# Kernel optimization log

Hardware: AMD Instinct MI355X
Metric: run time of the kernel (lower is better)

Reference implementation:

```python
import jax, jax.numpy as jnp
import numpy as np

DT = 0.1
DEATH_THRESHOLD = 0.05


def setup_inputs() -> dict:
    key = jax.random.key(0)
    ks = jax.random.split(key, 12)
    B, S, DE, DM, DC, DEPTH = 1, 4096, 256, 64, 64, 4
    DIN = DE + DC
    w_scale = 0.02  # keeps pre-softmax scores in a sane range
    return {
        "e": jax.random.normal(ks[0], (B, S, DE), jnp.float32),
        "E": jax.random.uniform(ks[1], (B, S, 1), jnp.float32),
        "P": jax.random.uniform(ks[2], (B, S, 1), jnp.float32),
        "G": jax.random.normal(ks[3], (B, S, 1), jnp.float32),
        "m": jax.random.uniform(ks[4], (B, S, DM), jnp.float32),
        "c": jax.random.normal(ks[5], (B, S, DC), jnp.float32),
        "l": jax.random.uniform(ks[6], (B, S, 1), jnp.float32),
        "wq": jax.random.normal(ks[7], (DEPTH, DIN, DE), jnp.float32) * w_scale,
        "bq": jnp.zeros((DEPTH, DE), jnp.float32),
        "wk": jax.random.normal(ks[8], (DEPTH, DIN, DE), jnp.float32) * w_scale,
        "bk": jnp.zeros((DEPTH, DE), jnp.float32),
        "wv": jax.random.normal(ks[9], (DEPTH, DIN, DE), jnp.float32) * w_scale,
        "bv": jnp.zeros((DEPTH, DE), jnp.float32),
        "alpha": jnp.full((DEPTH,), 1.0, jnp.float32),
        "beta": jnp.full((DEPTH,), 0.5, jnp.float32),
        "gamma": jnp.full((DEPTH,), 0.2, jnp.float32),
        "basal": jnp.full((DEPTH,), 0.05, jnp.float32),
    }


def reference(e, E, P, G, m, c, l, wq, bq, wk, bk, wv, bv, alpha, beta, gamma, basal):
    depth = wq.shape[0]
    scale = 1.0 / np.sqrt(wq.shape[-1]).astype(np.float32)
    for i in range(depth):
        # --- OuterTrans: multiplicatively-masked self-attention ---
        x = jnp.concatenate([e, c], axis=-1)                 # [B,S,DE+DC]
        q = x @ wq[i] + bq[i]
        k = x @ wk[i] + bk[i]
        v = x @ wv[i] + bv[i]
        scores = jnp.einsum("bsd,btd->bst", q, k) * scale    # [B,S,S]
        membrane = jnp.einsum("bsd,btd->bst", m, m)          # [B,S,S]
        lifespan = jnp.einsum("bsd,btd->bst", l, l)          # [B,S,S]
        attn = jax.nn.softmax(scores * membrane * lifespan, axis=-1)
        h_tilde = jnp.einsum("bst,btd->bsd", attn, v)        # [B,S,DE]
        e = e + h_tilde
        # --- ThermodynamicODE (elementwise per-token update) ---
        S_in = jnp.sum(h_tilde * h_tilde, axis=-1, keepdims=True)  # ||h||^2 [B,S,1]
        PE = P * E
        P_new = jax.nn.relu(P + (alpha[i] * S_in - beta[i] * PE) * DT)
        E_new = jax.nn.relu(E + (basal[i] - gamma[i] * PE) * DT)
        m_target = jax.nn.sigmoid(E_new - P_new)             # [B,S,1] broadcast to m
        G = G + (0.1 * E_new - 0.5 * P_new) * DT
        l_decay = 0.01 + 0.5 * jax.nn.relu(P_new - 2.0)
        m = 0.9 * m + 0.1 * m_target
        l = jnp.clip(l - l_decay * DT, 0.0, 1.0)
        E, P = E_new, P_new
    # Dynamic pruning: jit-compatible variant -> zero-mask dead cells instead of
    # data-dependent slicing; also return alive_mask and num_died.
    alive = l > DEATH_THRESHOLD                              # [B,S,1] bool
    af = alive.astype(e.dtype)
    num_died = e.shape[1] - jnp.sum(alive.astype(jnp.int32))
    return (e * af, E * af, P * af, G * af, m * af, c * af, l * af,
            alive[0, :, 0], num_died)
```

## Files before the change

### kernel.cpp

```cpp
#include <hip/hip_runtime.h>
#include <hip/hip_bf16.h>
#include <math.h>

#define SS 4096
#define DE 256
#define DM 64
#define DC 64
#define DIN 320
#define DEPTH 4
#define DT_C 0.1f
#define NSPLIT 12
#define BK 32
#define EXP_SHIFT 8.0f

typedef float f32x4_t __attribute__((ext_vector_type(4)));
typedef __bf16 bf16x8_t __attribute__((ext_vector_type(8)));

#define MFMA_BF16(A, B, C) __builtin_amdgcn_mfma_f32_16x16x32_bf16((A), (B), (C), 0, 0, 0)

#define OFF_E     (SS*DE)
#define OFF_P     (OFF_E + SS)
#define OFF_G     (OFF_P + SS)
#define OFF_M     (OFF_G + SS)
#define OFF_C     (OFF_M + SS*DM)
#define OFF_L     (OFF_C + SS*DM)
#define OFF_ALIVE (OFF_L + SS)
#define OFF_DIED  (OFF_ALIVE + SS)

#define WS_EWS   0
#define WS_MWS   (WS_EWS  + SS*DE)
#define WS_EE    (WS_MWS  + SS*DM)
#define WS_PP    (WS_EE   + SS)
#define WS_GG    (WS_PP   + SS)
#define WS_LL    (WS_GG   + SS)
#define WS_PL    (WS_LL   + SS)
#define WS_POB   (WS_PL   + NSPLIT*SS)
#define WS_XB    (WS_POB  + NSPLIT*SS*DE/2)
#define WS_QB    (WS_XB   + SS*DIN/2)
#define WS_KB    (WS_QB   + SS*DE/2)
#define WS_VTB   (WS_KB   + SS*DE/2)
#define WS_MB    (WS_VTB  + SS*DE/2)
#define WS_WT    (WS_MB   + SS*DM/2)

#define KT_STR 264
#define VT_STR 40

__global__ __launch_bounds__(256) void transpose_w_kernel(
    const float* __restrict__ wq, const float* __restrict__ wk, const float* __restrict__ wv,
    __hip_bfloat16* __restrict__ wt)
{
    const int zd = blockIdx.z;
    const int z = zd >> 2;
    const float* src = (z == 0 ? wq : (z == 1 ? wk : wv)) + (size_t)(zd & 3) * DIN * DE;
    __shared__ float t[32][33];
    const int k0 = blockIdx.x * 32;
    const int n0 = blockIdx.y * 32;
    const int tr = threadIdx.x >> 5;
    const int tc = threadIdx.x & 31;
    #pragma unroll
    for (int p = 0; p < 4; ++p)
        t[p*8 + tr][tc] = src[(size_t)(k0 + p*8 + tr) * DE + n0 + tc];
    __syncthreads();
    #pragma unroll
    for (int p = 0; p < 4; ++p) {
        int n = n0 + p*8 + tr;
        int k = k0 + tc;
        wt[((size_t)zd * DE + n) * DIN + k] = __float2bfloat16(t[tc][p*8 + tr]);
    }
}

__global__ __launch_bounds__(256) void init_kernel(
    const float* __restrict__ e_in, const float* __restrict__ c_in,
    const float* __restrict__ E_in, const float* __restrict__ P_in,
    const float* __restrict__ G_in, const float* __restrict__ l_in,
    const float* __restrict__ m_in,
    float* __restrict__ e_ws, __hip_bfloat16* __restrict__ xb,
    float* __restrict__ E_ws, float* __restrict__ P_ws, float* __restrict__ G_ws,
    float* __restrict__ l_ws, float* __restrict__ m_ws, __hip_bfloat16* __restrict__ mb)
{
    const int row = blockIdx.x;
    const int tid = threadIdx.x;
    const float v = e_in[(size_t)row * DE + tid];
    e_ws[(size_t)row * DE + tid] = v;
    xb[(size_t)row * DIN + tid] = __float2bfloat16(v);
    if (tid < DC) {
        xb[(size_t)row * DIN + DE + tid] = __float2bfloat16(c_in[(size_t)row * DC + tid]);
        const float mv = m_in[(size_t)row * DM + tid];
        m_ws[(size_t)row * DM + tid] = mv;
        mb[(size_t)row * DM + tid] = __float2bfloat16(mv);
    }
    if (tid == 0) {
        E_ws[row] = E_in[row];
        P_ws[row] = P_in[row];
        G_ws[row] = G_in[row];
        l_ws[row] = l_in[row];
    }
}

__global__ __launch_bounds__(256, 2) void proj_mfma_kernel(
    const __hip_bfloat16* __restrict__ xb, const __hip_bfloat16* __restrict__ wt,
    const float* __restrict__ bq, const float* __restrict__ bk, const float* __restrict__ bv,
    __hip_bfloat16* __restrict__ qb, __hip_bfloat16* __restrict__ kb, __hip_bfloat16* __restrict__ vtb,
    int layer)
{
    const int z = blockIdx.z;
    const int tid = threadIdx.x;
    const int w = tid >> 6, lane = tid & 63;
    const int m = lane & 15, quad = lane >> 4;
    const int row0 = blockIdx.x * 16;
    const __hip_bfloat16* wtz = wt + (size_t)(z * DEPTH + layer) * DE * DIN;
    const float* bias = (z == 0 ? bq : (z == 1 ? bk : bv)) + (size_t)layer * DE;

    bf16x8_t xa[10];
    #pragma unroll
    for (int kk = 0; kk < 10; ++kk)
        xa[kk] = *(const bf16x8_t*)&xb[(size_t)(row0 + m) * DIN + kk * 32 + quad * 8];

    f32x4_t acc[4];
    #pragma unroll
    for (int nt = 0; nt < 4; ++nt) acc[nt] = (f32x4_t){0.f, 0.f, 0.f, 0.f};

    #pragma unroll
    for (int kk = 0; kk < 10; ++kk) {
        #pragma unroll
        for (int nt = 0; nt < 4; ++nt) {
            const int ncol = w * 64 + nt * 16 + m;
            bf16x8_t bfrag = *(const bf16x8_t*)&wtz[(size_t)ncol * DIN + kk * 32 + quad * 8];
            acc[nt] = MFMA_BF16(xa[kk], bfrag, acc[nt]);
        }
    }
    #pragma unroll
    for (int nt = 0; nt < 4; ++nt) {
        const int col = w * 64 + nt * 16 + m;
        const float b = bias[col];
        #pragma unroll
        for (int r = 0; r < 4; ++r) {
            const int row = row0 + quad * 4 + r;
            const __hip_bfloat16 h = __float2bfloat16(acc[nt][r] + b);
            if (z == 0)      qb[(size_t)row * DE + col] = h;
            else if (z == 1) kb[(size_t)row * DE + col] = h;
            else             vtb[(size_t)col * SS + row] = h;
        }
    }
}

__global__ __launch_bounds__(256, 3) void attn_mfma_kernel(
    const __hip_bfloat16* __restrict__ qb, const __hip_bfloat16* __restrict__ kb,
    const __hip_bfloat16* __restrict__ vtb, const __hip_bfloat16* __restrict__ mb,
    const float* __restrict__ l_ws,
    __hip_bfloat16* __restrict__ part_ob, float* __restrict__ part_l)
{
    __shared__ __align__(16) __hip_bfloat16 kt[32 * KT_STR];
    __shared__ __align__(16) __hip_bfloat16 vt[256 * VT_STR];

    const int tid = threadIdx.x;
    const int w = tid >> 6, lane = tid & 63;
    const int n = lane & 15, quad = lane >> 4;
    const int row0 = blockIdx.x * 64 + w * 16;
    const int split = blockIdx.y;

    bf16x8_t qa[8];
    #pragma unroll
    for (int kk = 0; kk < 8; ++kk)
        qa[kk] = *(const bf16x8_t*)&qb[(size_t)(row0 + n) * DE + kk * 32 + quad * 8];
    bf16x8_t ma[2];
    #pragma unroll
    for (int kk = 0; kk < 2; ++kk)
        ma[kk] = *(const bf16x8_t*)&mb[(size_t)(row0 + n) * DM + kk * 32 + quad * 8];
    const float lqs = l_ws[row0 + n] * 0.0625f;

    f32x4_t oacc[16];
    #pragma unroll
    for (int ct = 0; ct < 16; ++ct) oacc[ct] = (f32x4_t){0.f, 0.f, 0.f, 0.f};
    float plsum = 0.f;
    const f32x4_t zf4 = (f32x4_t){0.f, 0.f, 0.f, 0.f};

    const int k_row = tid >> 5, k_g = tid & 31;
    const int v_col = tid >> 2, v_seg = tid & 3;
    const int v_base = (v_seg & 1) * 16 + (v_seg >> 1) * 4;

    const int it_begin = (split * 128) / NSPLIT;
    const int it_end   = ((split + 1) * 128) / NSPLIT;

    for (int it = it_begin; it < it_end; ++it) {
        const int t0 = it * BK;
        __syncthreads();
        #pragma unroll
        for (int p = 0; p < 4; ++p) {
            const int row = k_row + p * 8;
            *(float4*)&kt[row * KT_STR + k_g * 8] = *(const float4*)&kb[(size_t)(t0 + row) * DE + k_g * 8];
        }
        #pragma unroll
        for (int p = 0; p < 4; ++p) {
            const int col = v_col + p * 64;
            const float4 f = *(const float4*)&vtb[(size_t)col * SS + t0 + v_seg * 8];
            *(float2*)&vt[col * VT_STR + v_base]     = make_float2(f.x, f.y);
            *(float2*)&vt[col * VT_STR + v_base + 8] = make_float2(f.z, f.w);
        }
        __syncthreads();

        const bf16x8_t mf00 = *(const bf16x8_t*)&mb[(size_t)(t0 + n) * DM + quad * 8];
        const bf16x8_t mf01 = *(const bf16x8_t*)&mb[(size_t)(t0 + n) * DM + 32 + quad * 8];
        const bf16x8_t mf10 = *(const bf16x8_t*)&mb[(size_t)(t0 + n + 16) * DM + quad * 8];
        const bf16x8_t mf11 = *(const bf16x8_t*)&mb[(size_t)(t0 + n + 16) * DM + 32 + quad * 8];
        const float4 lk0 = *(const float4*)&l_ws[t0 + quad * 4];
        const float4 lk1 = *(const float4*)&l_ws[t0 + 16 + quad * 4];

        f32x4_t s0a = zf4, s0b = zf4, s1a = zf4, s1b = zf4;
        #pragma unroll
        for (int kk = 0; kk < 4; ++kk) {
            bf16x8_t k0 = *(const bf16x8_t*)&kt[n * KT_STR + kk * 32 + quad * 8];
            bf16x8_t k1 = *(const bf16x8_t*)&kt[(n + 16) * KT_STR + kk * 32 + quad * 8];
            s0a = MFMA_BF16(k0, qa[kk], s0a);
            s1a = MFMA_BF16(k1, qa[kk], s1a);
        }
        #pragma unroll
        for (int kk = 4; kk < 8; ++kk) {
            bf16x8_t k0 = *(const bf16x8_t*)&kt[n * KT_STR + kk * 32 + quad * 8];
            bf16x8_t k1 = *(const bf16x8_t*)&kt[(n + 16) * KT_STR + kk * 32 + quad * 8];
            s0b = MFMA_BF16(k0, qa[kk], s0b);
            s1b = MFMA_BF16(k1, qa[kk], s1b);
        }
        const f32x4_t st0 = s0a + s0b;
        const f32x4_t st1 = s1a + s1b;

        f32x4_t mm0 = MFMA_BF16(mf00, ma[0], zf4);
        mm0 = MFMA_BF16(mf01, ma[1], mm0);
        f32x4_t mm1 = MFMA_BF16(mf10, ma[0], zf4);
        mm1 = MFMA_BF16(mf11, ma[1], mm1);

        bf16x8_t pa;
        #pragma unroll
        for (int r = 0; r < 4; ++r) {
            const float x0 = st0[r] * lqs * lk0[r] * mm0[r];
            const float x1 = st1[r] * lqs * lk1[r] * mm1[r];
            const float p0 = __expf(x0 - EXP_SHIFT);
            const float p1 = __expf(x1 - EXP_SHIFT);
            plsum += p0 + p1;
            pa[r]     = (__bf16)p0;
            pa[4 + r] = (__bf16)p1;
        }

        #pragma unroll
        for (int ct = 0; ct < 16; ++ct) {
            bf16x8_t vb = *(const bf16x8_t*)&vt[(ct * 16 + n) * VT_STR + quad * 8];
            oacc[ct] = MFMA_BF16(pa, vb, oacc[ct]);
        }
    }

    plsum += __shfl_xor(plsum, 16);
    plsum += __shfl_xor(plsum, 32);
    if (lane < 16)
        part_l[split * SS + row0 + lane] = plsum;

    __hip_bfloat16* dst = part_ob + ((size_t)((split * (SS / 64) + blockIdx.x) * 4 + w)) * 4096;
    #pragma unroll
    for (int ct = 0; ct < 16; ++ct) {
        __hip_bfloat16 h4[4];
        #pragma unroll
        for (int r = 0; r < 4; ++r) h4[r] = __float2bfloat16(oacc[ct][r]);
        *(uint2*)&dst[(ct * 64 + lane) * 4] = *(uint2*)h4;
    }
}

__global__ __launch_bounds__(256) void fused_combine_kernel(
    const __hip_bfloat16* __restrict__ part_ob, const float* __restrict__ part_l,
    float* __restrict__ e_ws, __hip_bfloat16* __restrict__ xb,
    float* __restrict__ E_ws, float* __restrict__ P_ws, float* __restrict__ G_ws,
    float* __restrict__ m_ws, __hip_bfloat16* __restrict__ mb, float* __restrict__ l_ws,
    const float* __restrict__ alpha, const float* __restrict__ beta,
    const float* __restrict__ gamma_, const float* __restrict__ basal, int layer)
{
    const int wc = threadIdx.x >> 6, lane = threadIdx.x & 63;
    const int row = blockIdx.x * 4 + wc;
    const int qblk = row >> 6, wa = (row >> 4) & 3, quada = (row >> 2) & 3, ra = row & 3;

    float L = 0.f;
    #pragma unroll
    for (int s = 0; s < NSPLIT; ++s) L += part_l[s * SS + row];
    const float invL = 1.0f / L;

    const int ct = lane >> 2;
    const int base_off = (ct * 64 + quada * 16 + (lane & 3) * 4) * 4;
    float o[4] = {0.f, 0.f, 0.f, 0.f};
    #pragma unroll
    for (int s = 0; s < NSPLIT; ++s) {
        const size_t region = ((size_t)((s * (SS / 64) + qblk) * 4 + wa)) * 4096;
        const ushort* pp = (const ushort*)(part_ob + region) + base_off;
        ushort vals[16];
        *(uint4*)&vals[0] = *(const uint4*)pp;
        *(uint4*)&vals[8] = *(const uint4*)(pp + 8);
        #pragma unroll
        for (int j = 0; j < 4; ++j) {
            const unsigned u = vals[j * 4 + ra];
            o[j] += __uint_as_float(u << 16);
        }
    }
    float h0 = o[0] * invL, h1 = o[1] * invL, h2 = o[2] * invL, h3 = o[3] * invL;

    float4 ev = *(float4*)&e_ws[(size_t)row * DE + lane * 4];
    ev.x += h0; ev.y += h1; ev.z += h2; ev.w += h3;
    *(float4*)&e_ws[(size_t)row * DE + lane * 4] = ev;
    {
        __hip_bfloat16 x4[4] = {__float2bfloat16(ev.x), __float2bfloat16(ev.y),
                                __float2bfloat16(ev.z), __float2bfloat16(ev.w)};
        *(uint2*)&xb[(size_t)row * DIN + lane * 4] = *(uint2*)x4;
    }

    float ssq = h0*h0 + h1*h1 + h2*h2 + h3*h3;
    #pragma unroll
    for (int mask = 1; mask < 64; mask <<= 1) ssq += __shfl_xor(ssq, mask);

    const float a = alpha[layer], b = beta[layer], gm = gamma_[layer], bas = basal[layer];
    const float E = E_ws[row], P = P_ws[row];
    const float PE = P * E;
    const float Pn = fmaxf(0.f, P + (a * ssq - b * PE) * DT_C);
    const float En = fmaxf(0.f, E + (bas - gm * PE) * DT_C);
    const float mtg = 1.f / (1.f + __expf(-(En - Pn)));
    const size_t mi = (size_t)row * DM + lane;
    const float mv = 0.9f * m_ws[mi] + 0.1f * mtg;
    m_ws[mi] = mv;
    mb[mi] = __float2bfloat16(mv);
    if (lane == 0) {
        E_ws[row] = En;
        P_ws[row] = Pn;
        G_ws[row] = G_ws[row] + (0.1f * En - 0.5f * Pn) * DT_C;
        const float ldec = 0.01f + 0.5f * fmaxf(0.f, Pn - 2.0f);
        const float lv = l_ws[row] - ldec * DT_C;
        l_ws[row] = fminf(1.f, fmaxf(0.f, lv));
    }
}

__global__ __launch_bounds__(256) void finalize_kernel(
    const float* __restrict__ e_ws, const float* __restrict__ E_ws, const float* __restrict__ P_ws,
    const float* __restrict__ G_ws, const float* __restrict__ m_ws, const float* __restrict__ c,
    const float* __restrict__ l_ws, float* __restrict__ out)
{
    const int srow = blockIdx.x;
    const int tid = threadIdx.x;
    const float lv = l_ws[srow];
    const float af = (lv > 0.05f) ? 1.f : 0.f;
    out[(size_t)srow * DE + tid] = e_ws[(size_t)srow * DE + tid] * af;
    if (tid < DM) {
        out[OFF_M + (size_t)srow * DM + tid] = m_ws[(size_t)srow * DM + tid] * af;
        out[OFF_C + (size_t)srow * DM + tid] = c[(size_t)srow * DM + tid] * af;
    }
    if (tid == 0) {
        out[OFF_E + srow] = E_ws[srow] * af;
        out[OFF_P + srow] = P_ws[srow] * af;
        out[OFF_G + srow] = G_ws[srow] * af;
        out[OFF_L + srow] = lv * af;
        out[OFF_ALIVE + srow] = af;
    }
}

__global__ __launch_bounds__(256) void count_kernel(const float* __restrict__ l_ws, float* __restrict__ out)
{
    __shared__ float sdata[4];
    const int tid = threadIdx.x;
    int cnt = 0;
    for (int i = tid; i < SS; i += 256) cnt += (l_ws[i] > 0.05f) ? 1 : 0;
    float f = (float)cnt;
    #pragma unroll
    for (int mask = 1; mask < 64; mask <<= 1) f += __shfl_xor(f, mask);
    if ((tid & 63) == 0) sdata[tid >> 6] = f;
    __syncthreads();
    if (tid == 0) out[OFF_DIED] = (float)SS - (sdata[0] + sdata[1] + sdata[2] + sdata[3]);
}

extern "C" void kernel_launch(void* const* d_in, const int* in_sizes, int n_in,
                              void* d_out, int out_size, void* d_ws, size_t ws_size,
                              hipStream_t stream) {
    const float* e_in = (const float*)d_in[0];
    const float* E_in = (const float*)d_in[1];
    const float* P_in = (const float*)d_in[2];
    const float* G_in = (const float*)d_in[3];
    const float* m_in = (const float*)d_in[4];
    const float* c_in = (const float*)d_in[5];
    const float* l_in = (const float*)d_in[6];
    const float* wq = (const float*)d_in[7];
    const float* bq = (const float*)d_in[8];
    const float* wk = (const float*)d_in[9];
    const float* bk = (const float*)d_in[10];
    const float* wv = (const float*)d_in[11];
    const float* bv = (const float*)d_in[12];
    const float* alpha = (const float*)d_in[13];
    const float* beta  = (const float*)d_in[14];
    const float* gamma_ = (const float*)d_in[15];
    const float* basal = (const float*)d_in[16];
    float* out = (float*)d_out;
    float* ws = (float*)d_ws;

    float* e_ws = ws + WS_EWS;
    float* m_ws = ws + WS_MWS;
    float* E_ws = ws + WS_EE;
    float* P_ws = ws + WS_PP;
    float* G_ws = ws + WS_GG;
    float* l_ws = ws + WS_LL;
    float* part_l = ws + WS_PL;
    __hip_bfloat16* part_ob = (__hip_bfloat16*)(ws + WS_POB);
    __hip_bfloat16* xb  = (__hip_bfloat16*)(ws + WS_XB);
    __hip_bfloat16* qb  = (__hip_bfloat16*)(ws + WS_QB);
    __hip_bfloat16* kb  = (__hip_bfloat16*)(ws + WS_KB);
    __hip_bfloat16* vtb = (__hip_bfloat16*)(ws + WS_VTB);
    __hip_bfloat16* mb  = (__hip_bfloat16*)(ws + WS_MB);
    __hip_bfloat16* wt  = (__hip_bfloat16*)(ws + WS_WT);

    transpose_w_kernel<<<dim3(DIN/32, DE/32, 12), 256, 0, stream>>>(wq, wk, wv, wt);
    init_kernel<<<dim3(SS), 256, 0, stream>>>(
        e_in, c_in, E_in, P_in, G_in, l_in, m_in,
        e_ws, xb, E_ws, P_ws, G_ws, l_ws, m_ws, mb);

    for (int layer = 0; layer < DEPTH; ++layer) {
        proj_mfma_kernel<<<dim3(SS/16, 1, 3), 256, 0, stream>>>(
            xb, wt, bq, bk, bv, qb, kb, vtb, layer);
        attn_mfma_kernel<<<dim3(SS/64, NSPLIT), 256, 0, stream>>>(
            qb, kb, vtb, mb, l_ws, part_ob, part_l);
        fused_combine_kernel<<<dim3(SS/4), 256, 0, stream>>>(
            part_ob, part_l, e_ws, xb, E_ws, P_ws, G_ws, m_ws, mb, l_ws,
            alpha, beta, gamma_, basal, layer);
    }
    finalize_kernel<<<dim3(SS), 256, 0, stream>>>(
        e_ws, E_ws, P_ws, G_ws, m_ws, c_in, l_ws, out);
    count_kernel<<<1, 256, 0, stream>>>(l_ws, out);
}
```

Baseline: 466.0 us.

## Fuse combine into projection, merge QKV projections, fuse finalize and count

```diff
diff --git a/kernel.cpp b/kernel.cpp
--- a/kernel.cpp
+++ b/kernel.cpp
@@ -41,6 +41,7 @@
 #define WS_VTB   (WS_KB   + SS*DE/2)
 #define WS_MB    (WS_VTB  + SS*DE/2)
 #define WS_WT    (WS_MB   + SS*DM/2)
+#define WS_SEM   (WS_WT   + 3*DEPTH*DE*DIN/2)
 
 #define KT_STR 264
 #define VT_STR 40
@@ -76,7 +77,8 @@
     const float* __restrict__ m_in,
     float* __restrict__ e_ws, __hip_bfloat16* __restrict__ xb,
     float* __restrict__ E_ws, float* __restrict__ P_ws, float* __restrict__ G_ws,
-    float* __restrict__ l_ws, float* __restrict__ m_ws, __hip_bfloat16* __restrict__ mb)
+    float* __restrict__ l_ws, float* __restrict__ m_ws, __hip_bfloat16* __restrict__ mb,
+    int* __restrict__ counters)
 {
     const int row = blockIdx.x;
     const int tid = threadIdx.x;
@@ -95,43 +97,114 @@
         G_ws[row] = G_in[row];
         l_ws[row] = l_in[row];
     }
-}
-
-__global__ __launch_bounds__(256, 2) void proj_mfma_kernel(
-    const __hip_bfloat16* __restrict__ xb, const __hip_bfloat16* __restrict__ wt,
+    if (row == 0 && tid < 2) counters[tid] = 0;
+}
+
+__global__ __launch_bounds__(256, 2) void projc_kernel(
+    const __hip_bfloat16* __restrict__ part_ob, const float* __restrict__ part_l,
+    float* __restrict__ e_ws, __hip_bfloat16* __restrict__ xb,
+    float* __restrict__ E_ws, float* __restrict__ P_ws, float* __restrict__ G_ws,
+    float* __restrict__ m_ws, __hip_bfloat16* __restrict__ mb, float* __restrict__ l_ws,
+    const float* __restrict__ alpha, const float* __restrict__ beta,
+    const float* __restrict__ gamma_, const float* __restrict__ basal,
+    const __hip_bfloat16* __restrict__ wt,
     const float* __restrict__ bq, const float* __restrict__ bk, const float* __restrict__ bv,
     __hip_bfloat16* __restrict__ qb, __hip_bfloat16* __restrict__ kb, __hip_bfloat16* __restrict__ vtb,
     int layer)
 {
-    const int z = blockIdx.z;
+    const int id = blockIdx.x;
+    const int xcd = id & 7, inner = id >> 3;
+    const int qblk = (xcd << 3) | (inner >> 2);
+    const int rb = qblk * 4 + (inner & 3);
     const int tid = threadIdx.x;
+
+    if (layer > 0) {
+        const int wc = tid >> 6, lane = tid & 63;
+        const int lp = layer - 1;
+        const float a = alpha[lp], bb = beta[lp], gm = gamma_[lp], bas = basal[lp];
+        #pragma unroll
+        for (int rr = 0; rr < 4; ++rr) {
+            const int row = rb * 16 + wc * 4 + rr;
+            const int qb2 = row >> 6, wa = (row >> 4) & 3, quada = (row >> 2) & 3, ra = row & 3;
+            float L = 0.f;
+            #pragma unroll
+            for (int s = 0; s < NSPLIT; ++s) L += part_l[s * SS + row];
+            const float invL = 1.0f / L;
+            const int ct = lane >> 2;
+            const int base_off = (ct * 64 + quada * 16 + (lane & 3) * 4) * 4;
+            float o[4] = {0.f, 0.f, 0.f, 0.f};
+            #pragma unroll
+            for (int s = 0; s < NSPLIT; ++s) {
+                const size_t region = ((size_t)((s * (SS / 64) + qb2) * 4 + wa)) * 4096;
+                const ushort* pp = (const ushort*)(part_ob + region) + base_off;
+                ushort vals[16];
+                *(uint4*)&vals[0] = *(const uint4*)pp;
+                *(uint4*)&vals[8] = *(const uint4*)(pp + 8);
+                #pragma unroll
+                for (int j = 0; j < 4; ++j)
+                    o[j] += __uint_as_float(((unsigned)vals[j * 4 + ra]) << 16);
+            }
+            const float h0 = o[0] * invL, h1 = o[1] * invL, h2 = o[2] * invL, h3 = o[3] * invL;
+            float4 ev = *(float4*)&e_ws[(size_t)row * DE + lane * 4];
+            ev.x += h0; ev.y += h1; ev.z += h2; ev.w += h3;
+            *(float4*)&e_ws[(size_t)row * DE + lane * 4] = ev;
+            __hip_bfloat16 x4[4] = {__float2bfloat16(ev.x), __float2bfloat16(ev.y),
+                                    __float2bfloat16(ev.z), __float2bfloat16(ev.w)};
+            *(uint2*)&xb[(size_t)row * DIN + lane * 4] = *(uint2*)x4;
+
+            float ssq = h0*h0 + h1*h1 + h2*h2 + h3*h3;
+            #pragma unroll
+            for (int mask = 1; mask < 64; mask <<= 1) ssq += __shfl_xor(ssq, mask);
+
+            const float E = E_ws[row], P = P_ws[row];
+            const float PE = P * E;
+            const float Pn = fmaxf(0.f, P + (a * ssq - bb * PE) * DT_C);
+            const float En = fmaxf(0.f, E + (bas - gm * PE) * DT_C);
+            const float mtg = 1.f / (1.f + __expf(-(En - Pn)));
+            const size_t mi = (size_t)row * DM + lane;
+            const float mv = 0.9f * m_ws[mi] + 0.1f * mtg;
+            m_ws[mi] = mv;
+            mb[mi] = __float2bfloat16(mv);
+            if (lane == 0) {
+                E_ws[row] = En;
+                P_ws[row] = Pn;
+                G_ws[row] = G_ws[row] + (0.1f * En - 0.5f * Pn) * DT_C;
+                const float ldec = 0.01f + 0.5f * fmaxf(0.f, Pn - 2.0f);
+                const float lv = l_ws[row] - ldec * DT_C;
+                l_ws[row] = fminf(1.f, fmaxf(0.f, lv));
+            }
+        }
+        __syncthreads();
+    }
+
     const int w = tid >> 6, lane = tid & 63;
     const int m = lane & 15, quad = lane >> 4;
-    const int row0 = blockIdx.x * 16;
-    const __hip_bfloat16* wtz = wt + (size_t)(z * DEPTH + layer) * DE * DIN;
-    const float* bias = (z == 0 ? bq : (z == 1 ? bk : bv)) + (size_t)layer * DE;
+    const int row0 = rb * 16;
 
     bf16x8_t xa[10];
     #pragma unroll
     for (int kk = 0; kk < 10; ++kk)
         xa[kk] = *(const bf16x8_t*)&xb[(size_t)(row0 + m) * DIN + kk * 32 + quad * 8];
 
-    f32x4_t acc[4];
-    #pragma unroll
-    for (int nt = 0; nt < 4; ++nt) acc[nt] = (f32x4_t){0.f, 0.f, 0.f, 0.f};
+    f32x4_t acc[12];
+    #pragma unroll
+    for (int nt = 0; nt < 12; ++nt) acc[nt] = (f32x4_t){0.f, 0.f, 0.f, 0.f};
 
     #pragma unroll
     for (int kk = 0; kk < 10; ++kk) {
         #pragma unroll
-        for (int nt = 0; nt < 4; ++nt) {
-            const int ncol = w * 64 + nt * 16 + m;
-            bf16x8_t bfrag = *(const bf16x8_t*)&wtz[(size_t)ncol * DIN + kk * 32 + quad * 8];
+        for (int nt = 0; nt < 12; ++nt) {
+            const int gcol = w * 192 + nt * 16 + m;
+            const int z = gcol >> 8, col = gcol & 255;
+            bf16x8_t bfrag = *(const bf16x8_t*)&wt[((size_t)(z * DEPTH + layer) * DE + col) * DIN + kk * 32 + quad * 8];
             acc[nt] = MFMA_BF16(xa[kk], bfrag, acc[nt]);
         }
     }
     #pragma unroll
-    for (int nt = 0; nt < 4; ++nt) {
-        const int col = w * 64 + nt * 16 + m;
+    for (int nt = 0; nt < 12; ++nt) {
+        const int gcol = w * 192 + nt * 16 + m;
+        const int z = gcol >> 8, col = gcol & 255;
+        const float* bias = (z == 0 ? bq : (z == 1 ? bk : bv)) + (size_t)layer * DE;
         const float b = bias[col];
         #pragma unroll
         for (int r = 0; r < 4; ++r) {
@@ -153,11 +226,15 @@
     __shared__ __align__(16) __hip_bfloat16 kt[32 * KT_STR];
     __shared__ __align__(16) __hip_bfloat16 vt[256 * VT_STR];
 
+    const int id = blockIdx.x;
+    const int split = id >> 6;
+    const int rid = id & 63;
+    const int qblk = (rid & 7) * 8 + (rid >> 3);
+
     const int tid = threadIdx.x;
     const int w = tid >> 6, lane = tid & 63;
     const int n = lane & 15, quad = lane >> 4;
-    const int row0 = blockIdx.x * 64 + w * 16;
-    const int split = blockIdx.y;
+    const int row0 = qblk * 64 + w * 16;
 
     bf16x8_t qa[8];
     #pragma unroll
@@ -253,7 +330,7 @@
     if (lane < 16)
         part_l[split * SS + row0 + lane] = plsum;
 
-    __hip_bfloat16* dst = part_ob + ((size_t)((split * (SS / 64) + blockIdx.x) * 4 + w)) * 4096;
+    __hip_bfloat16* dst = part_ob + ((size_t)((split * (SS / 64) + qblk) * 4 + w)) * 4096;
     #pragma unroll
     for (int ct = 0; ct < 16; ++ct) {
         __hip_bfloat16 h4[4];
@@ -263,109 +340,96 @@
     }
 }
 
-__global__ __launch_bounds__(256) void fused_combine_kernel(
+__global__ __launch_bounds__(256) void finalizec_kernel(
     const __hip_bfloat16* __restrict__ part_ob, const float* __restrict__ part_l,
-    float* __restrict__ e_ws, __hip_bfloat16* __restrict__ xb,
-    float* __restrict__ E_ws, float* __restrict__ P_ws, float* __restrict__ G_ws,
-    float* __restrict__ m_ws, __hip_bfloat16* __restrict__ mb, float* __restrict__ l_ws,
+    const float* __restrict__ e_ws,
+    const float* __restrict__ E_ws, const float* __restrict__ P_ws, const float* __restrict__ G_ws,
+    const float* __restrict__ m_ws, const float* __restrict__ c_in, const float* __restrict__ l_ws,
     const float* __restrict__ alpha, const float* __restrict__ beta,
-    const float* __restrict__ gamma_, const float* __restrict__ basal, int layer)
+    const float* __restrict__ gamma_, const float* __restrict__ basal,
+    float* __restrict__ out, int* __restrict__ counters)
 {
-    const int wc = threadIdx.x >> 6, lane = threadIdx.x & 63;
-    const int row = blockIdx.x * 4 + wc;
-    const int qblk = row >> 6, wa = (row >> 4) & 3, quada = (row >> 2) & 3, ra = row & 3;
-
-    float L = 0.f;
-    #pragma unroll
-    for (int s = 0; s < NSPLIT; ++s) L += part_l[s * SS + row];
-    const float invL = 1.0f / L;
-
-    const int ct = lane >> 2;
-    const int base_off = (ct * 64 + quada * 16 + (lane & 3) * 4) * 4;
-    float o[4] = {0.f, 0.f, 0.f, 0.f};
-    #pragma unroll
-    for (int s = 0; s < NSPLIT; ++s) {
-        const size_t region = ((size_t)((s * (SS / 64) + qblk) * 4 + wa)) * 4096;
-        const ushort* pp = (const ushort*)(part_ob + region) + base_off;
-        ushort vals[16];
-        *(uint4*)&vals[0] = *(const uint4*)pp;
-        *(uint4*)&vals[8] = *(const uint4*)(pp + 8);
-        #pragma unroll
-        for (int j = 0; j < 4; ++j) {
-            const unsigned u = vals[j * 4 + ra];
-            o[j] += __uint_as_float(u << 16);
-        }
-    }
-    float h0 = o[0] * invL, h1 = o[1] * invL, h2 = o[2] * invL, h3 = o[3] * invL;
-
-    float4 ev = *(float4*)&e_ws[(size_t)row * DE + lane * 4];
-    ev.x += h0; ev.y += h1; ev.z += h2; ev.w += h3;
-    *(float4*)&e_ws[(size_t)row * DE + lane * 4] = ev;
-    {
-        __hip_bfloat16 x4[4] = {__float2bfloat16(ev.x), __float2bfloat16(ev.y),
-                                __float2bfloat16(ev.z), __float2bfloat16(ev.w)};
-        *(uint2*)&xb[(size_t)row * DIN + lane * 4] = *(uint2*)x4;
-    }
-
-    float ssq = h0*h0 + h1*h1 + h2*h2 + h3*h3;
-    #pragma unroll
-    for (int mask = 1; mask < 64; mask <<= 1) ssq += __shfl_xor(ssq, mask);
-
-    const float a = alpha[layer], b = beta[layer], gm = gamma_[layer], bas = basal[layer];
-    const float E = E_ws[row], P = P_ws[row];
-    const float PE = P * E;
-    const float Pn = fmaxf(0.f, P + (a * ssq - b * PE) * DT_C);
-    const float En = fmaxf(0.f, E + (bas - gm * PE) * DT_C);
-    const float mtg = 1.f / (1.f + __expf(-(En - Pn)));
-    const size_t mi = (size_t)row * DM + lane;
-    const float mv = 0.9f * m_ws[mi] + 0.1f * mtg;
-    m_ws[mi] = mv;
-    mb[mi] = __float2bfloat16(mv);
-    if (lane == 0) {
-        E_ws[row] = En;
-        P_ws[row] = Pn;
-        G_ws[row] = G_ws[row] + (0.1f * En - 0.5f * Pn) * DT_C;
+    const int id = blockIdx.x;
+    const int xcd = id & 7, inner = id >> 3;
+    const int qblk = (xcd << 3) | (inner >> 2);
+    const int rb = qblk * 4 + (inner & 3);
+    const int tid = threadIdx.x;
+    const int wc = tid >> 6, lane = tid & 63;
+
+    const int lp = DEPTH - 1;
+    const float a = alpha[lp], bb = beta[lp], gm = gamma_[lp], bas = basal[lp];
+
+    __shared__ int s_alive[4];
+    int alive_cnt = 0;
+
+    #pragma unroll
+    for (int rr = 0; rr < 4; ++rr) {
+        const int row = rb * 16 + wc * 4 + rr;
+        const int qb2 = row >> 6, wa = (row >> 4) & 3, quada = (row >> 2) & 3, ra = row & 3;
+        float L = 0.f;
+        #pragma unroll
+        for (int s = 0; s < NSPLIT; ++s) L += part_l[s * SS + row];
+        const float invL = 1.0f / L;
+        const int ct = lane >> 2;
+        const int base_off = (ct * 64 + quada * 16 + (lane & 3) * 4) * 4;
+        float o[4] = {0.f, 0.f, 0.f, 0.f};
+        #pragma unroll
+        for (int s = 0; s < NSPLIT; ++s) {
+            const size_t region = ((size_t)((s * (SS / 64) + qb2) * 4 + wa)) * 4096;
+            const ushort* pp = (const ushort*)(part_ob + region) + base_off;
+            ushort vals[16];
+            *(uint4*)&vals[0] = *(const uint4*)pp;
+            *(uint4*)&vals[8] = *(const uint4*)(pp + 8);
+            #pragma unroll
+            for (int j = 0; j < 4; ++j)
+                o[j] += __uint_as_float(((unsigned)vals[j * 4 + ra]) << 16);
+        }
+        const float h0 = o[0] * invL, h1 = o[1] * invL, h2 = o[2] * invL, h3 = o[3] * invL;
+        float4 ev = *(const float4*)&e_ws[(size_t)row * DE + lane * 4];
+        ev.x += h0; ev.y += h1; ev.z += h2; ev.w += h3;
+
+        float ssq = h0*h0 + h1*h1 + h2*h2 + h3*h3;
+        #pragma unroll
+        for (int mask = 1; mask < 64; mask <<= 1) ssq += __shfl_xor(ssq, mask);
+
+        const float E = E_ws[row], P = P_ws[row];
+        const float PE = P * E;
+        const float Pn = fmaxf(0.f, P + (a * ssq - bb * PE) * DT_C);
+        const float En = fmaxf(0.f, E + (bas - gm * PE) * DT_C);
+        const float mtg = 1.f / (1.f + __expf(-(En - Pn)));
+        const float mv = 0.9f * m_ws[(size_t)row * DM + lane] + 0.1f * mtg;
+        const float Gn = G_ws[row] + (0.1f * En - 0.5f * Pn) * DT_C;
         const float ldec = 0.01f + 0.5f * fmaxf(0.f, Pn - 2.0f);
-        const float lv = l_ws[row] - ldec * DT_C;
-        l_ws[row] = fminf(1.f, fmaxf(0.f, lv));
-    }
-}
-
-__global__ __launch_bounds__(256) void finalize_kernel(
-    const float* __restrict__ e_ws, const float* __restrict__ E_ws, const float* __restrict__ P_ws,
-    const float* __restrict__ G_ws, const float* __restrict__ m_ws, const float* __restrict__ c,
-    const float* __restrict__ l_ws, float* __restrict__ out)
-{
-    const int srow = blockIdx.x;
-    const int tid = threadIdx.x;
-    const float lv = l_ws[srow];
-    const float af = (lv > 0.05f) ? 1.f : 0.f;
-    out[(size_t)srow * DE + tid] = e_ws[(size_t)srow * DE + tid] * af;
-    if (tid < DM) {
-        out[OFF_M + (size_t)srow * DM + tid] = m_ws[(size_t)srow * DM + tid] * af;
-        out[OFF_C + (size_t)srow * DM + tid] = c[(size_t)srow * DM + tid] * af;
-    }
+        const float lv = fminf(1.f, fmaxf(0.f, l_ws[row] - ldec * DT_C));
+        const float af = (lv > 0.05f) ? 1.f : 0.f;
+
+        float4 eo = make_float4(ev.x * af, ev.y * af, ev.z * af, ev.w * af);
+        *(float4*)&out[(size_t)row * DE + lane * 4] = eo;
+        out[OFF_M + (size_t)row * DM + lane] = mv * af;
+        out[OFF_C + (size_t)row * DM + lane] = c_in[(size_t)row * DM + lane] * af;
+        if (lane == 0) {
+            out[OFF_E + row] = En * af;
+            out[OFF_P + row] = Pn * af;
+            out[OFF_G + row] = Gn * af;
+            out[OFF_L + row] = lv * af;
+            out[OFF_ALIVE + row] = af;
+            alive_cnt += (af > 0.f) ? 1 : 0;
+        }
+    }
+
+    if (lane == 0) s_alive[wc] = alive_cnt;
+    __syncthreads();
     if (tid == 0) {
-        out[OFF_E + srow] = E_ws[srow] * af;
-        out[OFF_P + srow] = P_ws[srow] * af;
-        out[OFF_G + srow] = G_ws[srow] * af;
-        out[OFF_L + srow] = lv * af;
-        out[OFF_ALIVE + srow] = af;
-    }
-}
-
-__global__ __launch_bounds__(256) void count_kernel(const float* __restrict__ l_ws, float* __restrict__ out)
-{
-    __shared__ float sdata[4];
-    const int tid = threadIdx.x;
-    int cnt = 0;
-    for (int i = tid; i < SS; i += 256) cnt += (l_ws[i] > 0.05f) ? 1 : 0;
-    float f = (float)cnt;
-    #pragma unroll
-    for (int mask = 1; mask < 64; mask <<= 1) f += __shfl_xor(f, mask);
-    if ((tid & 63) == 0) sdata[tid >> 6] = f;
-    __syncthreads();
-    if (tid == 0) out[OFF_DIED] = (float)SS - (sdata[0] + sdata[1] + sdata[2] + sdata[3]);
+        const int blk_alive = s_alive[0] + s_alive[1] + s_alive[2] + s_alive[3];
+        atomicAdd(&counters[0], blk_alive);
+        __threadfence();
+        const int old = atomicAdd(&counters[1], 1);
+        if (old == 255) {
+            __threadfence();
+            const int tot = atomicAdd(&counters[0], 0);
+            out[OFF_DIED] = (float)(SS - tot);
+        }
+    }
 }
 
 extern "C" void kernel_launch(void* const* d_in, const int* in_sizes, int n_in,
@@ -405,22 +469,21 @@
     __hip_bfloat16* vtb = (__hip_bfloat16*)(ws + WS_VTB);
     __hip_bfloat16* mb  = (__hip_bfloat16*)(ws + WS_MB);
     __hip_bfloat16* wt  = (__hip_bfloat16*)(ws + WS_WT);
+    int* counters = (int*)(ws + WS_SEM);
 
     transpose_w_kernel<<<dim3(DIN/32, DE/32, 12), 256, 0, stream>>>(wq, wk, wv, wt);
     init_kernel<<<dim3(SS), 256, 0, stream>>>(
         e_in, c_in, E_in, P_in, G_in, l_in, m_in,
-        e_ws, xb, E_ws, P_ws, G_ws, l_ws, m_ws, mb);
+        e_ws, xb, E_ws, P_ws, G_ws, l_ws, m_ws, mb, counters);
 
     for (int layer = 0; layer < DEPTH; ++layer) {
-        proj_mfma_kernel<<<dim3(SS/16, 1, 3), 256, 0, stream>>>(
-            xb, wt, bq, bk, bv, qb, kb, vtb, layer);
-        attn_mfma_kernel<<<dim3(SS/64, NSPLIT), 256, 0, stream>>>(
+        projc_kernel<<<dim3(SS/16), 256, 0, stream>>>(
+            part_ob, part_l, e_ws, xb, E_ws, P_ws, G_ws, m_ws, mb, l_ws,
+            alpha, beta, gamma_, basal, wt, bq, bk, bv, qb, kb, vtb, layer);
+        attn_mfma_kernel<<<dim3((SS/64) * NSPLIT), 256, 0, stream>>>(
             qb, kb, vtb, mb, l_ws, part_ob, part_l);
-        fused_combine_kernel<<<dim3(SS/4), 256, 0, stream>>>(
-            part_ob, part_l, e_ws, xb, E_ws, P_ws, G_ws, m_ws, mb, l_ws,
-            alpha, beta, gamma_, basal, layer);
-    }
-    finalize_kernel<<<dim3(SS), 256, 0, stream>>>(
-        e_ws, E_ws, P_ws, G_ws, m_ws, c_in, l_ws, out);
-    count_kernel<<<1, 256, 0, stream>>>(l_ws, out);
-}
+    }
+    finalizec_kernel<<<dim3(SS/16), 256, 0, stream>>>(
+        part_ob, part_l, e_ws, E_ws, P_ws, G_ws, m_ws, c_in, l_ws,
+        alpha, beta, gamma_, basal, out, counters);
+}
```

Result: no change. 469.6 us (+0.8%).
